# Kernel optimization log

Measured on AMD Instinct MI355X. Metric: run time of the kernel, lower is better.

Reference implementation:

```python
import jax, jax.numpy as jnp
import numpy as np

D_MODEL = 2048
N_HEADS = 16
N_KV_HEADS = 4
HEAD_DIM = 128
ROPE_THETA = 1000000.0
B, T = 2, 2048


def setup_inputs() -> dict:
    key = jax.random.key(0)
    ks = jax.random.split(key, 5)
    s_in = 1.0 / np.sqrt(D_MODEL)
    s_o = 1.0 / np.sqrt(N_HEADS * HEAD_DIM)
    return {
        "x": jax.random.normal(ks[0], (B, T, D_MODEL), jnp.float32),
        "w_q": jax.random.normal(ks[1], (N_HEADS * HEAD_DIM, D_MODEL), jnp.float32) * s_in,
        "w_k": jax.random.normal(ks[2], (N_KV_HEADS * HEAD_DIM, D_MODEL), jnp.float32) * s_in,
        "w_v": jax.random.normal(ks[3], (N_KV_HEADS * HEAD_DIM, D_MODEL), jnp.float32) * s_in,
        "w_o": jax.random.normal(ks[4], (D_MODEL, N_HEADS * HEAD_DIM), jnp.float32) * s_o,
    }


def _rope_cos_sin(T, dtype):
    # inv_freq over even dims, emb = concat(freqs, freqs) (HF/llama convention)
    inv_freq = 1.0 / (ROPE_THETA ** (jnp.arange(0, HEAD_DIM, 2, dtype=jnp.float32) / HEAD_DIM))
    freqs = jnp.arange(T, dtype=jnp.float32)[:, None] * inv_freq[None, :]  # [T, hd/2]
    emb = jnp.concatenate([freqs, freqs], axis=-1)  # [T, hd]
    return jnp.cos(emb).astype(dtype), jnp.sin(emb).astype(dtype)


def _rotate_half(x):
    x1, x2 = jnp.split(x, 2, axis=-1)
    return jnp.concatenate([-x2, x1], axis=-1)


def reference(x, w_q, w_k, w_v, w_o):
    B, T, D = x.shape
    # QKV projections (bias=False), split heads -> [B, H, T, hd]
    q = (x @ w_q.T).reshape(B, T, N_HEADS, HEAD_DIM).transpose(0, 2, 1, 3)
    k = (x @ w_k.T).reshape(B, T, N_KV_HEADS, HEAD_DIM).transpose(0, 2, 1, 3)
    v = (x @ w_v.T).reshape(B, T, N_KV_HEADS, HEAD_DIM).transpose(0, 2, 1, 3)
    # RoPE
    cos, sin = _rope_cos_sin(T, x.dtype)  # [T, hd]
    q = q * cos + _rotate_half(q) * sin
    k = k * cos + _rotate_half(k) * sin
    # GQA: expand kv heads (repeat_interleave over head dim)
    rep = N_HEADS // N_KV_HEADS
    k = jnp.repeat(k, rep, axis=1)
    v = jnp.repeat(v, rep, axis=1)
    # Eager attention: QK^T * scale + causal mask, softmax, PV
    scale = HEAD_DIM ** -0.5
    scores = jnp.einsum("bhtd,bhsd->bhts", q, k) * scale
    causal = jnp.tril(jnp.ones((T, T), dtype=bool))
    scores = jnp.where(causal[None, None], scores, jnp.finfo(scores.dtype).min)
    probs = jax.nn.softmax(scores, axis=-1)
    out = jnp.einsum("bhts,bhsd->bhtd", probs, v)  # [B, H, T, hd]
    out = out.transpose(0, 2, 1, 3).reshape(B, T, N_HEADS * HEAD_DIM)
    return out @ w_o.T
```

## Files before the change

kernel.cpp:

```cpp
#include <hip/hip_runtime.h>
#include <cstdint>
#include <cstddef>

typedef unsigned short u16;
typedef unsigned u32;
typedef unsigned long long u64;
typedef __attribute__((ext_vector_type(8))) short short8;
typedef __attribute__((ext_vector_type(4))) float f32x4;

#define T_SEQ 2048
#define DM    2048
#define NHEAD 16
#define NKV   4
#define HD    128
#define NEGBIG (-3.0e38f)
#define QSCALE 0.1275525165017459f
#define L2IF (-0.31143258583318043f)

__device__ __forceinline__ u16 f2bf(float f) {
  union { float f; unsigned u; } c; c.f = f;
  return (u16)((c.u + 0x7fffu + ((c.u >> 16) & 1u)) >> 16);
}
__device__ __forceinline__ float bf2f(u16 b) {
  union { float f; unsigned u; } c; c.u = ((unsigned)b) << 16;
  return c.f;
}
__device__ __forceinline__ void gl_lds16(const u16* g, u16* l) {
  __builtin_amdgcn_global_load_lds(
      (const __attribute__((address_space(1))) void*)g,
      (__attribute__((address_space(3))) void*)l, 16, 0, 0);
}

__global__ void castk_all(const float* __restrict__ x, const float* __restrict__ wq,
                          const float* __restrict__ wk, const float* __restrict__ wv,
                          const float* __restrict__ wo, u16* __restrict__ dst) {
  long long i4 = (long long)blockIdx.x * 256 + threadIdx.x;
  const float* src; long long off;
  if (i4 < (2LL << 20))                    { src = x;  off = i4; }
  else if (i4 < (3LL << 20))               { src = wq; off = i4 - (2LL << 20); }
  else if (i4 < (3LL << 20) + (1 << 18))   { src = wk; off = i4 - (3LL << 20); }
  else if (i4 < (3LL << 20) + (2 << 18))   { src = wv; off = i4 - (3LL << 20) - (1 << 18); }
  else                                     { src = wo; off = i4 - (3LL << 20) - (2 << 18); }
  float4 v = *(const float4*)(src + off * 4);
  u16* d = dst + i4 * 4;
  d[0] = f2bf(v.x); d[1] = f2bf(v.y); d[2] = f2bf(v.z); d[3] = f2bf(v.w);
}

__global__ void tabk(float2* __restrict__ Tab) {
  int idx = blockIdx.x * 256 + threadIdx.x;
  float ang = (float)(idx >> 6) * exp2f((float)(idx & 63) * L2IF);
  float sn, cs;
  sincosf(ang, &sn, &cs);
  Tab[idx] = make_float2(cs, sn);
}

__global__ void ropek(u16* __restrict__ buf, const float2* __restrict__ Tab) {
  int idx = blockIdx.x * 256 + threadIdx.x;
  int r = idx >> 6, i = idx & 63;
  int t = r & (T_SEQ - 1);
  float2 cs = Tab[(t << 6) + i];
  size_t base = (size_t)r * HD + i;
  float x1 = bf2f(buf[base]), x2 = bf2f(buf[base + 64]);
  buf[base]      = f2bf(x1 * cs.x - x2 * cs.y);
  buf[base + 64] = f2bf(x2 * cs.x + x1 * cs.y);
}

template <int MODE>
__global__ __launch_bounds__(256) void gemm_bt(
    const u16* __restrict__ A, const u16* __restrict__ Bm,
    void* __restrict__ Out0, u16* __restrict__ OutK, u16* __restrict__ OutV,
    int M, int N, int K) {
  __shared__ __align__(16) u16 As[2][128 * 32];
  __shared__ __align__(16) u16 Bs[2][128 * 32];
  const int tid = threadIdx.x;
  const int w = tid >> 6, l = tid & 63;
  const int lm = l & 15, q = l >> 4;
  const int chunk = gridDim.x >> 3;
  const int nid = (blockIdx.x & 7) * chunk + (blockIdx.x >> 3);
  const int nbx = N >> 7;
  const int by = nid / nbx, bx = nid - by * nbx;
  const int m0 = by * 128, n0 = bx * 128;
  const int mq = w & 1, nq = w >> 1;
  const u16* Ab = A + (size_t)m0 * K;
  const u16* Bb = Bm + (size_t)n0 * K;

  const int s0_ = w * 64 + l, s1_ = 256 + s0_;
  const int row0 = s0_ >> 2, sc0 = (((s0_ & 3) ^ ((s0_ >> 3) & 3))) * 8;
  const int row1 = s1_ >> 2, sc1 = (((s1_ & 3) ^ ((s1_ >> 3) & 3))) * 8;
  const int rs = (lm >> 1) & 3;

  f32x4 acc[4][4] = {};
  const int nk = K >> 5;

  gl_lds16(Ab + (size_t)row0 * K + sc0, &As[0][s0_ * 8]);
  gl_lds16(Bb + (size_t)row0 * K + sc0, &Bs[0][s0_ * 8]);
  gl_lds16(Ab + (size_t)row1 * K + sc1, &As[0][s1_ * 8]);
  gl_lds16(Bb + (size_t)row1 * K + sc1, &Bs[0][s1_ * 8]);
  __syncthreads();

  for (int ki = 0; ki < nk; ++ki) {
    const int bb = ki & 1;
    if (ki + 1 < nk) {
      const int k0 = (ki + 1) << 5;
      gl_lds16(Ab + (size_t)row0 * K + k0 + sc0, &As[bb ^ 1][s0_ * 8]);
      gl_lds16(Bb + (size_t)row0 * K + k0 + sc0, &Bs[bb ^ 1][s0_ * 8]);
      gl_lds16(Ab + (size_t)row1 * K + k0 + sc1, &As[bb ^ 1][s1_ * 8]);
      gl_lds16(Bb + (size_t)row1 * K + k0 + sc1, &Bs[bb ^ 1][s1_ * 8]);
    }
    short8 af[4], bf[4];
#pragma unroll
    for (int i = 0; i < 4; ++i) {
      af[i] = *(const short8*)(&As[bb][(mq * 64 + i * 16 + lm) * 32 + (q ^ rs) * 8]);
      bf[i] = *(const short8*)(&Bs[bb][(nq * 64 + i * 16 + lm) * 32 + (q ^ rs) * 8]);
    }
#pragma unroll
    for (int i = 0; i < 4; ++i)
#pragma unroll
      for (int j = 0; j < 4; ++j)
        acc[i][j] = __builtin_amdgcn_mfma_f32_16x16x32_bf16(af[i], bf[j], acc[i][j], 0, 0, 0);
    __syncthreads();
  }

#pragma unroll
  for (int i = 0; i < 4; ++i)
#pragma unroll
    for (int j = 0; j < 4; ++j)
#pragma unroll
      for (int r = 0; r < 4; ++r) {
        int m = m0 + mq * 64 + i * 16 + q * 4 + r;
        int n = n0 + nq * 64 + j * 16 + lm;
        float v = acc[i][j][r];
        if constexpr (MODE == 0) {
          ((float*)Out0)[(size_t)m * N + n] = v;
        } else {
          int b = m >> 11, t = m & (T_SEQ - 1);
          if (n < 2048) {
            int h = n >> 7, d = n & (HD - 1);
            ((u16*)Out0)[(((size_t)(b * NHEAD + h)) * T_SEQ + t) * HD + d] = f2bf(v * QSCALE);
          } else if (n < 2560) {
            int nn = n - 2048, h = nn >> 7, d = nn & (HD - 1);
            OutK[(((size_t)(b * NKV + h)) * T_SEQ + t) * HD + d] = f2bf(v);
          } else {
            int nn = n - 2560, h = nn >> 7, d = nn & (HD - 1);
            OutV[(((size_t)(b * NKV + h)) * HD + d) * T_SEQ + t] = f2bf(v);
          }
        }
      }
}

#define PSTRIDE 72
__global__ __launch_bounds__(256, 2) void attnk(
    const u16* __restrict__ Q, const u16* __restrict__ Kh,
    const u16* __restrict__ Vt, const float2* __restrict__ Tab,
    u16* __restrict__ Oa) {
  __shared__ __align__(16) u16 Ks[2][64 * 128];
  __shared__ __align__(16) u16 Vs[2][128 * 64];
  __shared__ __align__(16) u16 Pl[4][16 * PSTRIDE];
  const int tid = threadIdx.x;
  const int w = tid >> 6, l = tid & 63, lm = l & 15, q = l >> 4;

  const int wg = blockIdx.x;
  const int g = wg & 7, slot = wg >> 3;
  const int b = g >> 2, kvh = g & 3;
  const int h = kvh * 4 + (slot & 3);
  const int p = slot >> 2;

  const u16* Kb = Kh + ((size_t)(b * NKV + kvh)) * T_SEQ * HD;
  const u16* Vb = Vt + ((size_t)(b * NKV + kvh)) * HD * T_SEQ;
  u16* Pw = Pl[w];

  const int r16 = tid >> 4, c16 = tid & 15;
  const int r8  = tid >> 3, c8  = tid & 7;

#pragma unroll 1
  for (int half = 0; half < 2; ++half) {
    const int tile = half ? p : (31 - p);
    const int tbase = tile * 64 + w * 16;
    const u16* Qb = Q + (((size_t)(b * NHEAD + h)) * T_SEQ + tbase) * HD;

    short8 qa[4];
#pragma unroll
    for (int ks = 0; ks < 4; ++ks)
      qa[ks] = *(const short8*)(Qb + (size_t)lm * HD + ks * 32 + q * 8);

    {
      const float2* tb = Tab + (((size_t)(tbase + lm)) << 6) + q * 8;
#pragma unroll
      for (int ks = 0; ks < 2; ++ks) {
        short8 lo = qa[ks], hi = qa[ks + 2];
#pragma unroll
        for (int e = 0; e < 8; ++e) {
          float2 cs = tb[ks * 32 + e];
          float x1 = bf2f((u16)lo[e]), x2 = bf2f((u16)hi[e]);
          lo[e] = (short)f2bf(x1 * cs.x - x2 * cs.y);
          hi[e] = (short)f2bf(x2 * cs.x + x1 * cs.y);
        }
        qa[ks] = lo; qa[ks + 2] = hi;
      }
    }

    float m_i = NEGBIG, l_i = 0.f;
    f32x4 oacc[8] = {};
    const int nst = tile + 1;

    {
#pragma unroll
      for (int j = 0; j < 4; ++j) {
        int s = j * 16 + r16, gs = c16 ^ (s & 15);
        gl_lds16(Kb + (size_t)s * HD + gs * 8, &Ks[0][s * 128 + c16 * 8]);
      }
#pragma unroll
      for (int j = 0; j < 4; ++j) {
        int d = j * 32 + r8, gs = c8 ^ (d & 7);
        gl_lds16(Vb + (size_t)d * T_SEQ + gs * 8, &Vs[0][d * 64 + c8 * 8]);
      }
    }
    __syncthreads();

    for (int st = 0; st < nst; ++st) {
      const int bb = st & 1;
      if (st + 1 < nst) {
        const int s0n = (st + 1) * 64;
#pragma unroll
        for (int j = 0; j < 4; ++j) {
          int s = j * 16 + r16, gs = c16 ^ (s & 15);
          gl_lds16(Kb + (size_t)(s0n + s) * HD + gs * 8, &Ks[bb ^ 1][s * 128 + c16 * 8]);
        }
#pragma unroll
        for (int j = 0; j < 4; ++j) {
          int d = j * 32 + r8, gs = c8 ^ (d & 7);
          gl_lds16(Vb + (size_t)d * T_SEQ + s0n + gs * 8, &Vs[bb ^ 1][d * 64 + c8 * 8]);
        }
      }

      f32x4 sacc[4] = {};
#pragma unroll
      for (int ks = 0; ks < 4; ++ks)
#pragma unroll
        for (int nt = 0; nt < 4; ++nt) {
          short8 kb = *(const short8*)(&Ks[bb][(nt * 16 + lm) * 128 + ((ks * 4 + q) ^ lm) * 8]);
          sacc[nt] = __builtin_amdgcn_mfma_f32_16x16x32_bf16(kb, qa[ks], sacc[nt], 0, 0, 0);
        }

      const bool diag = (st == nst - 1);
      const int s0 = st * 64;
      float mx = NEGBIG;
#pragma unroll
      for (int nt = 0; nt < 4; ++nt)
#pragma unroll
        for (int j = 0; j < 4; ++j) {
          float v = sacc[nt][j];
          if (diag) {
            int s_abs = s0 + nt * 16 + q * 4 + j;
            if (s_abs > tbase + lm) v = NEGBIG;
            sacc[nt][j] = v;
          }
          mx = fmaxf(mx, v);
        }
      mx = fmaxf(mx, __shfl_xor(mx, 16, 64));
      mx = fmaxf(mx, __shfl_xor(mx, 32, 64));
      if (__any(mx > m_i + 8.0f)) {
        float mnew = fmaxf(m_i, mx);
        float alpha = exp2f(m_i - mnew);
        m_i = mnew;
        l_i *= alpha;
#pragma unroll
        for (int dt = 0; dt < 8; ++dt)
#pragma unroll
          for (int j = 0; j < 4; ++j) oacc[dt][j] *= alpha;
      }
      float sum = 0.f;
#pragma unroll
      for (int nt = 0; nt < 4; ++nt) {
        float e0 = exp2f(sacc[nt][0] - m_i), e1 = exp2f(sacc[nt][1] - m_i);
        float e2 = exp2f(sacc[nt][2] - m_i), e3 = exp2f(sacc[nt][3] - m_i);
        sum += (e0 + e1) + (e2 + e3);
        u32 lo32 = __builtin_amdgcn_perm(__float_as_uint(e1), __float_as_uint(e0), 0x07060302u);
        u32 hi32 = __builtin_amdgcn_perm(__float_as_uint(e3), __float_as_uint(e2), 0x07060302u);
        *(u64*)(Pw + lm * PSTRIDE + nt * 16 + q * 4) = ((u64)hi32 << 32) | lo32;
      }
      sum += __shfl_xor(sum, 16, 64);
      sum += __shfl_xor(sum, 32, 64);
      l_i += sum;

      asm volatile("" ::: "memory");

#pragma unroll
      for (int ks = 0; ks < 2; ++ks) {
        short8 pa = *(const short8*)(Pw + lm * PSTRIDE + ks * 32 + q * 8);
#pragma unroll
        for (int dt = 0; dt < 8; ++dt) {
          short8 vb = *(const short8*)(
              &Vs[bb][(dt * 16 + lm) * 64 + ((ks * 4 + q) ^ (lm & 7)) * 8]);
          oacc[dt] = __builtin_amdgcn_mfma_f32_16x16x32_bf16(vb, pa, oacc[dt], 0, 0, 0);
        }
      }
      __syncthreads();
    }

    float inv = 1.0f / l_i;
    int t = tbase + lm;
#pragma unroll
    for (int dt = 0; dt < 8; ++dt) {
      u16 ok[4];
#pragma unroll
      for (int j = 0; j < 4; ++j) ok[j] = f2bf(oacc[dt][j] * inv);
      *(u64*)(Oa + ((size_t)(b * T_SEQ + t)) * (NHEAD * HD) + h * HD + dt * 16 + q * 4) =
          (u64)ok[0] | ((u64)ok[1] << 16) | ((u64)ok[2] << 32) | ((u64)ok[3] << 48);
    }
  }
}

extern "C" void kernel_launch(void* const* d_in, const int* in_sizes, int n_in,
                              void* d_out, int out_size, void* d_ws, size_t ws_size,
                              hipStream_t stream) {
  const float* x  = (const float*)d_in[0];
  const float* wq = (const float*)d_in[1];
  const float* wk = (const float*)d_in[2];
  const float* wv = (const float*)d_in[3];
  const float* wo = (const float*)d_in[4];
  float* out = (float*)d_out;

  u16* ws  = (u16*)d_ws;
  u16* xb  = ws;
  u16* wqb = xb  + (8u << 20);
  u16* wkb = wqb + (4u << 20);
  u16* wvb = wkb + (1u << 20);
  u16* wob = wvb + (1u << 20);
  u16* Qb  = wob + (4u << 20);
  u16* Kb  = Qb  + (8u << 20);
  u16* Vtb = Kb  + (2u << 20);
  u16* Ab  = xb;
  float2* tab = (float2*)wkb;

  castk_all<<<18432, 256, 0, stream>>>(x, wq, wk, wv, wo, ws);

  gemm_bt<3><<<768, 256, 0, stream>>>(xb, wqb, Qb, Kb, Vtb, 4096, 3072, 2048);

  tabk<<<512, 256, 0, stream>>>(tab);
  ropek<<<4096, 256, 0, stream>>>(Kb, tab);

  attnk<<<512, 256, 0, stream>>>(Qb, Kb, Vtb, tab, Ab);

  gemm_bt<0><<<512, 256, 0, stream>>>(Ab, wob, out, nullptr, nullptr, 4096, 2048, 2048);
}
```

Measured before the change: 291.3 us.

## Split attention into one tile per block with smaller KV blocks and fuse rope table

The attention kernel no longer pairs a long and a short query tile per block. It now launches one block per query tile (1024 blocks), uses 32-row KV stages with smaller LDS buffers, and raises the occupancy hint to 4 blocks per CU, with swizzle and P-stride reworked to match. The separate RoPE table kernel is folded into the K-rope kernel, which computes sin/cos inline and writes the table for the attention kernel. The aims are more parallelism and occupancy plus one fewer launch. The cost is load imbalance from causal tiles of different lengths, and twice as many sync and softmax steps per unit of work.

```diff
diff --git a/kernel.cpp b/kernel.cpp
--- a/kernel.cpp
+++ b/kernel.cpp
@@ -46,23 +46,18 @@
   d[0] = f2bf(v.x); d[1] = f2bf(v.y); d[2] = f2bf(v.z); d[3] = f2bf(v.w);
 }
 
-__global__ void tabk(float2* __restrict__ Tab) {
-  int idx = blockIdx.x * 256 + threadIdx.x;
-  float ang = (float)(idx >> 6) * exp2f((float)(idx & 63) * L2IF);
-  float sn, cs;
-  sincosf(ang, &sn, &cs);
-  Tab[idx] = make_float2(cs, sn);
-}
-
-__global__ void ropek(u16* __restrict__ buf, const float2* __restrict__ Tab) {
+__global__ void ropek(u16* __restrict__ buf, float2* __restrict__ Tab) {
   int idx = blockIdx.x * 256 + threadIdx.x;
   int r = idx >> 6, i = idx & 63;
   int t = r & (T_SEQ - 1);
-  float2 cs = Tab[(t << 6) + i];
+  float ang = (float)t * exp2f((float)i * L2IF);
+  float sn, cs;
+  sincosf(ang, &sn, &cs);
+  if (r < T_SEQ) Tab[(r << 6) + i] = make_float2(cs, sn);
   size_t base = (size_t)r * HD + i;
   float x1 = bf2f(buf[base]), x2 = bf2f(buf[base + 64]);
-  buf[base]      = f2bf(x1 * cs.x - x2 * cs.y);
-  buf[base + 64] = f2bf(x2 * cs.x + x1 * cs.y);
+  buf[base]      = f2bf(x1 * cs - x2 * sn);
+  buf[base + 64] = f2bf(x2 * cs + x1 * sn);
 }
 
 template <int MODE>
@@ -148,13 +143,14 @@
       }
 }
 
-#define PSTRIDE 72
-__global__ __launch_bounds__(256, 2) void attnk(
+#define KVB 32
+#define PSTRIDE 40
+__global__ __launch_bounds__(256, 4) void attnk(
     const u16* __restrict__ Q, const u16* __restrict__ Kh,
     const u16* __restrict__ Vt, const float2* __restrict__ Tab,
     u16* __restrict__ Oa) {
-  __shared__ __align__(16) u16 Ks[2][64 * 128];
-  __shared__ __align__(16) u16 Vs[2][128 * 64];
+  __shared__ __align__(16) u16 Ks[2][KVB * 128];
+  __shared__ __align__(16) u16 Vs[2][128 * KVB];
   __shared__ __align__(16) u16 Pl[4][16 * PSTRIDE];
   const int tid = threadIdx.x;
   const int w = tid >> 6, l = tid & 63, lm = l & 15, q = l >> 4;
@@ -163,151 +159,136 @@
   const int g = wg & 7, slot = wg >> 3;
   const int b = g >> 2, kvh = g & 3;
   const int h = kvh * 4 + (slot & 3);
-  const int p = slot >> 2;
+  const int tile = 31 - (slot >> 2);
 
   const u16* Kb = Kh + ((size_t)(b * NKV + kvh)) * T_SEQ * HD;
   const u16* Vb = Vt + ((size_t)(b * NKV + kvh)) * HD * T_SEQ;
   u16* Pw = Pl[w];
 
-  const int r16 = tid >> 4, c16 = tid & 15;
-  const int r8  = tid >> 3, c8  = tid & 7;
-
-#pragma unroll 1
-  for (int half = 0; half < 2; ++half) {
-    const int tile = half ? p : (31 - p);
-    const int tbase = tile * 64 + w * 16;
-    const u16* Qb = Q + (((size_t)(b * NHEAD + h)) * T_SEQ + tbase) * HD;
-
-    short8 qa[4];
+  const int krow = tid >> 4;
+  const int kc   = tid & 15;
+  const int kcol = (kc ^ (krow & 15)) * 8;
+  const int vrow = tid >> 2;
+  const int vc   = tid & 3;
+  const int vcol = (vc ^ ((tid >> 3) & 3)) * 8;
+
+  const int tbase = tile * 64 + w * 16;
+  const u16* Qb = Q + (((size_t)(b * NHEAD + h)) * T_SEQ + tbase) * HD;
+
+  short8 qa[4];
+#pragma unroll
+  for (int ks = 0; ks < 4; ++ks)
+    qa[ks] = *(const short8*)(Qb + (size_t)lm * HD + ks * 32 + q * 8);
+
+  {
+    const float2* tb = Tab + (((size_t)(tbase + lm)) << 6) + q * 8;
+#pragma unroll
+    for (int ks = 0; ks < 2; ++ks) {
+      short8 lo = qa[ks], hi = qa[ks + 2];
+#pragma unroll
+      for (int e = 0; e < 8; ++e) {
+        float2 cs = tb[ks * 32 + e];
+        float x1 = bf2f((u16)lo[e]), x2 = bf2f((u16)hi[e]);
+        lo[e] = (short)f2bf(x1 * cs.x - x2 * cs.y);
+        hi[e] = (short)f2bf(x2 * cs.x + x1 * cs.y);
+      }
+      qa[ks] = lo; qa[ks + 2] = hi;
+    }
+  }
+
+  float m_i = NEGBIG, l_i = 0.f;
+  f32x4 oacc[8] = {};
+  const int nst = 2 * tile + 2;
+
+  gl_lds16(Kb + (size_t)krow * HD + kcol, &Ks[0][krow * 128 + kc * 8]);
+  gl_lds16(Kb + (size_t)(krow + 16) * HD + kcol, &Ks[0][(krow + 16) * 128 + kc * 8]);
+  gl_lds16(Vb + (size_t)vrow * T_SEQ + vcol, &Vs[0][vrow * KVB + vc * 8]);
+  gl_lds16(Vb + (size_t)(vrow + 64) * T_SEQ + vcol, &Vs[0][(vrow + 64) * KVB + vc * 8]);
+  __syncthreads();
+
+  for (int st = 0; st < nst; ++st) {
+    const int bb = st & 1;
+    const int s0 = st * KVB;
+    if (st + 1 < nst) {
+      const int s0n = s0 + KVB;
+      gl_lds16(Kb + (size_t)(s0n + krow) * HD + kcol, &Ks[bb ^ 1][krow * 128 + kc * 8]);
+      gl_lds16(Kb + (size_t)(s0n + krow + 16) * HD + kcol, &Ks[bb ^ 1][(krow + 16) * 128 + kc * 8]);
+      gl_lds16(Vb + (size_t)vrow * T_SEQ + s0n + vcol, &Vs[bb ^ 1][vrow * KVB + vc * 8]);
+      gl_lds16(Vb + (size_t)(vrow + 64) * T_SEQ + s0n + vcol, &Vs[bb ^ 1][(vrow + 64) * KVB + vc * 8]);
+    }
+
+    f32x4 sacc[2] = {};
 #pragma unroll
     for (int ks = 0; ks < 4; ++ks)
-      qa[ks] = *(const short8*)(Qb + (size_t)lm * HD + ks * 32 + q * 8);
+#pragma unroll
+      for (int nt = 0; nt < 2; ++nt) {
+        short8 kb = *(const short8*)(&Ks[bb][(nt * 16 + lm) * 128 + ((ks * 4 + q) ^ lm) * 8]);
+        sacc[nt] = __builtin_amdgcn_mfma_f32_16x16x32_bf16(kb, qa[ks], sacc[nt], 0, 0, 0);
+      }
+
+    const bool diag = (s0 + KVB - 1 > tbase);
+    float mx = NEGBIG;
+#pragma unroll
+    for (int nt = 0; nt < 2; ++nt)
+#pragma unroll
+      for (int j = 0; j < 4; ++j) {
+        float v = sacc[nt][j];
+        if (diag) {
+          int s_abs = s0 + nt * 16 + q * 4 + j;
+          if (s_abs > tbase + lm) v = NEGBIG;
+          sacc[nt][j] = v;
+        }
+        mx = fmaxf(mx, v);
+      }
+    mx = fmaxf(mx, __shfl_xor(mx, 16, 64));
+    mx = fmaxf(mx, __shfl_xor(mx, 32, 64));
+    if (__any(mx > m_i + 8.0f)) {
+      float mnew = fmaxf(m_i, mx);
+      float alpha = exp2f(m_i - mnew);
+      m_i = mnew;
+      l_i *= alpha;
+#pragma unroll
+      for (int dt = 0; dt < 8; ++dt)
+#pragma unroll
+        for (int j = 0; j < 4; ++j) oacc[dt][j] *= alpha;
+    }
+    float sum = 0.f;
+#pragma unroll
+    for (int nt = 0; nt < 2; ++nt) {
+      float e0 = exp2f(sacc[nt][0] - m_i), e1 = exp2f(sacc[nt][1] - m_i);
+      float e2 = exp2f(sacc[nt][2] - m_i), e3 = exp2f(sacc[nt][3] - m_i);
+      sum += (e0 + e1) + (e2 + e3);
+      u32 lo32 = __builtin_amdgcn_perm(__float_as_uint(e1), __float_as_uint(e0), 0x07060302u);
+      u32 hi32 = __builtin_amdgcn_perm(__float_as_uint(e3), __float_as_uint(e2), 0x07060302u);
+      *(u64*)(Pw + lm * PSTRIDE + nt * 16 + q * 4) = ((u64)hi32 << 32) | lo32;
+    }
+    sum += __shfl_xor(sum, 16, 64);
+    sum += __shfl_xor(sum, 32, 64);
+    l_i += sum;
+
+    asm volatile("" ::: "memory");
 
     {
-      const float2* tb = Tab + (((size_t)(tbase + lm)) << 6) + q * 8;
-#pragma unroll
-      for (int ks = 0; ks < 2; ++ks) {
-        short8 lo = qa[ks], hi = qa[ks + 2];
-#pragma unroll
-        for (int e = 0; e < 8; ++e) {
-          float2 cs = tb[ks * 32 + e];
-          float x1 = bf2f((u16)lo[e]), x2 = bf2f((u16)hi[e]);
-          lo[e] = (short)f2bf(x1 * cs.x - x2 * cs.y);
-          hi[e] = (short)f2bf(x2 * cs.x + x1 * cs.y);
-        }
-        qa[ks] = lo; qa[ks + 2] = hi;
-      }
-    }
-
-    float m_i = NEGBIG, l_i = 0.f;
-    f32x4 oacc[8] = {};
-    const int nst = tile + 1;
-
-    {
-#pragma unroll
-      for (int j = 0; j < 4; ++j) {
-        int s = j * 16 + r16, gs = c16 ^ (s & 15);
-        gl_lds16(Kb + (size_t)s * HD + gs * 8, &Ks[0][s * 128 + c16 * 8]);
-      }
-#pragma unroll
-      for (int j = 0; j < 4; ++j) {
-        int d = j * 32 + r8, gs = c8 ^ (d & 7);
-        gl_lds16(Vb + (size_t)d * T_SEQ + gs * 8, &Vs[0][d * 64 + c8 * 8]);
+      short8 pa = *(const short8*)(Pw + lm * PSTRIDE + q * 8);
+#pragma unroll
+      for (int dt = 0; dt < 8; ++dt) {
+        short8 vb = *(const short8*)(
+            &Vs[bb][(dt * 16 + lm) * KVB + (q ^ ((lm >> 1) & 3)) * 8]);
+        oacc[dt] = __builtin_amdgcn_mfma_f32_16x16x32_bf16(vb, pa, oacc[dt], 0, 0, 0);
       }
     }
     __syncthreads();
-
-    for (int st = 0; st < nst; ++st) {
-      const int bb = st & 1;
-      if (st + 1 < nst) {
-        const int s0n = (st + 1) * 64;
-#pragma unroll
-        for (int j = 0; j < 4; ++j) {
-          int s = j * 16 + r16, gs = c16 ^ (s & 15);
-          gl_lds16(Kb + (size_t)(s0n + s) * HD + gs * 8, &Ks[bb ^ 1][s * 128 + c16 * 8]);
-        }
-#pragma unroll
-        for (int j = 0; j < 4; ++j) {
-          int d = j * 32 + r8, gs = c8 ^ (d & 7);
-          gl_lds16(Vb + (size_t)d * T_SEQ + s0n + gs * 8, &Vs[bb ^ 1][d * 64 + c8 * 8]);
-        }
-      }
-
-      f32x4 sacc[4] = {};
-#pragma unroll
-      for (int ks = 0; ks < 4; ++ks)
-#pragma unroll
-        for (int nt = 0; nt < 4; ++nt) {
-          short8 kb = *(const short8*)(&Ks[bb][(nt * 16 + lm) * 128 + ((ks * 4 + q) ^ lm) * 8]);
-          sacc[nt] = __builtin_amdgcn_mfma_f32_16x16x32_bf16(kb, qa[ks], sacc[nt], 0, 0, 0);
-        }
-
-      const bool diag = (st == nst - 1);
-      const int s0 = st * 64;
-      float mx = NEGBIG;
-#pragma unroll
-      for (int nt = 0; nt < 4; ++nt)
-#pragma unroll
-        for (int j = 0; j < 4; ++j) {
-          float v = sacc[nt][j];
-          if (diag) {
-            int s_abs = s0 + nt * 16 + q * 4 + j;
-            if (s_abs > tbase + lm) v = NEGBIG;
-            sacc[nt][j] = v;
-          }
-          mx = fmaxf(mx, v);
-        }
-      mx = fmaxf(mx, __shfl_xor(mx, 16, 64));
-      mx = fmaxf(mx, __shfl_xor(mx, 32, 64));
-      if (__any(mx > m_i + 8.0f)) {
-        float mnew = fmaxf(m_i, mx);
-        float alpha = exp2f(m_i - mnew);
-        m_i = mnew;
-        l_i *= alpha;
-#pragma unroll
-        for (int dt = 0; dt < 8; ++dt)
-#pragma unroll
-          for (int j = 0; j < 4; ++j) oacc[dt][j] *= alpha;
-      }
-      float sum = 0.f;
-#pragma unroll
-      for (int nt = 0; nt < 4; ++nt) {
-        float e0 = exp2f(sacc[nt][0] - m_i), e1 = exp2f(sacc[nt][1] - m_i);
-        float e2 = exp2f(sacc[nt][2] - m_i), e3 = exp2f(sacc[nt][3] - m_i);
-        sum += (e0 + e1) + (e2 + e3);
-        u32 lo32 = __builtin_amdgcn_perm(__float_as_uint(e1), __float_as_uint(e0), 0x07060302u);
-        u32 hi32 = __builtin_amdgcn_perm(__float_as_uint(e3), __float_as_uint(e2), 0x07060302u);
-        *(u64*)(Pw + lm * PSTRIDE + nt * 16 + q * 4) = ((u64)hi32 << 32) | lo32;
-      }
-      sum += __shfl_xor(sum, 16, 64);
-      sum += __shfl_xor(sum, 32, 64);
-      l_i += sum;
-
-      asm volatile("" ::: "memory");
-
-#pragma unroll
-      for (int ks = 0; ks < 2; ++ks) {
-        short8 pa = *(const short8*)(Pw + lm * PSTRIDE + ks * 32 + q * 8);
-#pragma unroll
-        for (int dt = 0; dt < 8; ++dt) {
-          short8 vb = *(const short8*)(
-              &Vs[bb][(dt * 16 + lm) * 64 + ((ks * 4 + q) ^ (lm & 7)) * 8]);
-          oacc[dt] = __builtin_amdgcn_mfma_f32_16x16x32_bf16(vb, pa, oacc[dt], 0, 0, 0);
-        }
-      }
-      __syncthreads();
-    }
-
-    float inv = 1.0f / l_i;
-    int t = tbase + lm;
-#pragma unroll
-    for (int dt = 0; dt < 8; ++dt) {
-      u16 ok[4];
-#pragma unroll
-      for (int j = 0; j < 4; ++j) ok[j] = f2bf(oacc[dt][j] * inv);
-      *(u64*)(Oa + ((size_t)(b * T_SEQ + t)) * (NHEAD * HD) + h * HD + dt * 16 + q * 4) =
-          (u64)ok[0] | ((u64)ok[1] << 16) | ((u64)ok[2] << 32) | ((u64)ok[3] << 48);
-    }
+  }
+
+  float inv = 1.0f / l_i;
+  int t = tbase + lm;
+#pragma unroll
+  for (int dt = 0; dt < 8; ++dt) {
+    u16 ok[4];
+#pragma unroll
+    for (int j = 0; j < 4; ++j) ok[j] = f2bf(oacc[dt][j] * inv);
+    *(u64*)(Oa + ((size_t)(b * T_SEQ + t)) * (NHEAD * HD) + h * HD + dt * 16 + q * 4) =
+        (u64)ok[0] | ((u64)ok[1] << 16) | ((u64)ok[2] << 32) | ((u64)ok[3] << 48);
   }
 }
 
@@ -337,10 +318,9 @@
 
   gemm_bt<3><<<768, 256, 0, stream>>>(xb, wqb, Qb, Kb, Vtb, 4096, 3072, 2048);
 
-  tabk<<<512, 256, 0, stream>>>(tab);
   ropek<<<4096, 256, 0, stream>>>(Kb, tab);
 
-  attnk<<<512, 256, 0, stream>>>(Qb, Kb, Vtb, tab, Ab);
+  attnk<<<1024, 256, 0, stream>>>(Qb, Kb, Vtb, tab, Ab);
 
   gemm_bt<0><<<512, 256, 0, stream>>>(Ab, wob, out, nullptr, nullptr, 4096, 2048, 2048);
 }
```

Result: slower. 305.0 us (+4.7%).

## Give each attention wave 32 query rows and fold RoPE table build into ropek

Applied to the files above, without the earlier changes.

The attention kernel now runs 128-thread blocks of two waves, and each wave processes two 16-row query groups, so every K and V fragment read from LDS feeds two MFMAs. The intent is to halve LDS traffic per unit of compute. The cost is doubled accumulator registers (oacc and sacc) and fewer waves per block to hide latency. Separately, the sin/cos table is now computed inside the K RoPE kernel, which writes the table for the first 2048 rows, removing one launch.

```diff
diff --git a/kernel.cpp b/kernel.cpp
--- a/kernel.cpp
+++ b/kernel.cpp
@@ -46,23 +46,18 @@
   d[0] = f2bf(v.x); d[1] = f2bf(v.y); d[2] = f2bf(v.z); d[3] = f2bf(v.w);
 }
 
-__global__ void tabk(float2* __restrict__ Tab) {
-  int idx = blockIdx.x * 256 + threadIdx.x;
-  float ang = (float)(idx >> 6) * exp2f((float)(idx & 63) * L2IF);
-  float sn, cs;
-  sincosf(ang, &sn, &cs);
-  Tab[idx] = make_float2(cs, sn);
-}
-
-__global__ void ropek(u16* __restrict__ buf, const float2* __restrict__ Tab) {
+__global__ void ropek(u16* __restrict__ buf, float2* __restrict__ Tab) {
   int idx = blockIdx.x * 256 + threadIdx.x;
   int r = idx >> 6, i = idx & 63;
   int t = r & (T_SEQ - 1);
-  float2 cs = Tab[(t << 6) + i];
+  float ang = (float)t * exp2f((float)i * L2IF);
+  float sn, cs;
+  sincosf(ang, &sn, &cs);
+  if (r < T_SEQ) Tab[(r << 6) + i] = make_float2(cs, sn);
   size_t base = (size_t)r * HD + i;
   float x1 = bf2f(buf[base]), x2 = bf2f(buf[base + 64]);
-  buf[base]      = f2bf(x1 * cs.x - x2 * cs.y);
-  buf[base + 64] = f2bf(x2 * cs.x + x1 * cs.y);
+  buf[base]      = f2bf(x1 * cs - x2 * sn);
+  buf[base + 64] = f2bf(x2 * cs + x1 * sn);
 }
 
 template <int MODE>
@@ -149,13 +144,13 @@
 }
 
 #define PSTRIDE 72
-__global__ __launch_bounds__(256, 2) void attnk(
+__global__ __launch_bounds__(128) void attnk(
     const u16* __restrict__ Q, const u16* __restrict__ Kh,
     const u16* __restrict__ Vt, const float2* __restrict__ Tab,
     u16* __restrict__ Oa) {
   __shared__ __align__(16) u16 Ks[2][64 * 128];
   __shared__ __align__(16) u16 Vs[2][128 * 64];
-  __shared__ __align__(16) u16 Pl[4][16 * PSTRIDE];
+  __shared__ __align__(16) u16 Pl[2][32 * PSTRIDE];
   const int tid = threadIdx.x;
   const int w = tid >> 6, l = tid & 63, lm = l & 15, q = l >> 4;
 
@@ -175,19 +170,23 @@
 #pragma unroll 1
   for (int half = 0; half < 2; ++half) {
     const int tile = half ? p : (31 - p);
-    const int tbase = tile * 64 + w * 16;
-    const u16* Qb = Q + (((size_t)(b * NHEAD + h)) * T_SEQ + tbase) * HD;
-
-    short8 qa[4];
-#pragma unroll
-    for (int ks = 0; ks < 4; ++ks)
-      qa[ks] = *(const short8*)(Qb + (size_t)lm * HD + ks * 32 + q * 8);
-
-    {
-      const float2* tb = Tab + (((size_t)(tbase + lm)) << 6) + q * 8;
+    const int tbase = tile * 64;
+    const int qrb = tbase + w * 32;
+    const u16* Qb = Q + (((size_t)(b * NHEAD + h)) * T_SEQ + qrb) * HD;
+
+    short8 qa[2][4];
+#pragma unroll
+    for (int rg = 0; rg < 2; ++rg)
+#pragma unroll
+      for (int ks = 0; ks < 4; ++ks)
+        qa[rg][ks] = *(const short8*)(Qb + (size_t)(rg * 16 + lm) * HD + ks * 32 + q * 8);
+
+#pragma unroll
+    for (int rg = 0; rg < 2; ++rg) {
+      const float2* tb = Tab + (((size_t)(qrb + rg * 16 + lm)) << 6) + q * 8;
 #pragma unroll
       for (int ks = 0; ks < 2; ++ks) {
-        short8 lo = qa[ks], hi = qa[ks + 2];
+        short8 lo = qa[rg][ks], hi = qa[rg][ks + 2];
 #pragma unroll
         for (int e = 0; e < 8; ++e) {
           float2 cs = tb[ks * 32 + e];
@@ -195,118 +194,132 @@
           lo[e] = (short)f2bf(x1 * cs.x - x2 * cs.y);
           hi[e] = (short)f2bf(x2 * cs.x + x1 * cs.y);
         }
-        qa[ks] = lo; qa[ks + 2] = hi;
-      }
-    }
-
-    float m_i = NEGBIG, l_i = 0.f;
-    f32x4 oacc[8] = {};
+        qa[rg][ks] = lo; qa[rg][ks + 2] = hi;
+      }
+    }
+
+    float m_i[2] = {NEGBIG, NEGBIG}, l_i[2] = {0.f, 0.f};
+    f32x4 oacc[2][8] = {};
     const int nst = tile + 1;
 
-    {
-#pragma unroll
-      for (int j = 0; j < 4; ++j) {
-        int s = j * 16 + r16, gs = c16 ^ (s & 15);
-        gl_lds16(Kb + (size_t)s * HD + gs * 8, &Ks[0][s * 128 + c16 * 8]);
-      }
-#pragma unroll
-      for (int j = 0; j < 4; ++j) {
-        int d = j * 32 + r8, gs = c8 ^ (d & 7);
-        gl_lds16(Vb + (size_t)d * T_SEQ + gs * 8, &Vs[0][d * 64 + c8 * 8]);
-      }
+#pragma unroll
+    for (int j = 0; j < 8; ++j) {
+      int s = j * 8 + r16, gs = c16 ^ (s & 15);
+      gl_lds16(Kb + (size_t)s * HD + gs * 8, &Ks[0][s * 128 + c16 * 8]);
+    }
+#pragma unroll
+    for (int j = 0; j < 8; ++j) {
+      int d = j * 16 + r8, gs = c8 ^ (d & 7);
+      gl_lds16(Vb + (size_t)d * T_SEQ + gs * 8, &Vs[0][d * 64 + c8 * 8]);
     }
     __syncthreads();
 
     for (int st = 0; st < nst; ++st) {
       const int bb = st & 1;
+      const int s0 = st * 64;
       if (st + 1 < nst) {
-        const int s0n = (st + 1) * 64;
-#pragma unroll
-        for (int j = 0; j < 4; ++j) {
-          int s = j * 16 + r16, gs = c16 ^ (s & 15);
+        const int s0n = s0 + 64;
+#pragma unroll
+        for (int j = 0; j < 8; ++j) {
+          int s = j * 8 + r16, gs = c16 ^ (s & 15);
           gl_lds16(Kb + (size_t)(s0n + s) * HD + gs * 8, &Ks[bb ^ 1][s * 128 + c16 * 8]);
         }
 #pragma unroll
-        for (int j = 0; j < 4; ++j) {
-          int d = j * 32 + r8, gs = c8 ^ (d & 7);
+        for (int j = 0; j < 8; ++j) {
+          int d = j * 16 + r8, gs = c8 ^ (d & 7);
           gl_lds16(Vb + (size_t)d * T_SEQ + s0n + gs * 8, &Vs[bb ^ 1][d * 64 + c8 * 8]);
         }
       }
 
-      f32x4 sacc[4] = {};
+      f32x4 sacc[2][4] = {};
 #pragma unroll
       for (int ks = 0; ks < 4; ++ks)
 #pragma unroll
         for (int nt = 0; nt < 4; ++nt) {
           short8 kb = *(const short8*)(&Ks[bb][(nt * 16 + lm) * 128 + ((ks * 4 + q) ^ lm) * 8]);
-          sacc[nt] = __builtin_amdgcn_mfma_f32_16x16x32_bf16(kb, qa[ks], sacc[nt], 0, 0, 0);
-        }
-
-      const bool diag = (st == nst - 1);
-      const int s0 = st * 64;
-      float mx = NEGBIG;
-#pragma unroll
-      for (int nt = 0; nt < 4; ++nt)
-#pragma unroll
-        for (int j = 0; j < 4; ++j) {
-          float v = sacc[nt][j];
-          if (diag) {
-            int s_abs = s0 + nt * 16 + q * 4 + j;
-            if (s_abs > tbase + lm) v = NEGBIG;
-            sacc[nt][j] = v;
+          sacc[0][nt] = __builtin_amdgcn_mfma_f32_16x16x32_bf16(kb, qa[0][ks], sacc[0][nt], 0, 0, 0);
+          sacc[1][nt] = __builtin_amdgcn_mfma_f32_16x16x32_bf16(kb, qa[1][ks], sacc[1][nt], 0, 0, 0);
+        }
+
+      const bool diag = (s0 + 63 > qrb);
+      float mx[2] = {NEGBIG, NEGBIG};
+#pragma unroll
+      for (int rg = 0; rg < 2; ++rg) {
+#pragma unroll
+        for (int nt = 0; nt < 4; ++nt)
+#pragma unroll
+          for (int j = 0; j < 4; ++j) {
+            float v = sacc[rg][nt][j];
+            if (diag) {
+              int s_abs = s0 + nt * 16 + q * 4 + j;
+              if (s_abs > qrb + rg * 16 + lm) v = NEGBIG;
+              sacc[rg][nt][j] = v;
+            }
+            mx[rg] = fmaxf(mx[rg], v);
           }
-          mx = fmaxf(mx, v);
-        }
-      mx = fmaxf(mx, __shfl_xor(mx, 16, 64));
-      mx = fmaxf(mx, __shfl_xor(mx, 32, 64));
-      if (__any(mx > m_i + 8.0f)) {
-        float mnew = fmaxf(m_i, mx);
-        float alpha = exp2f(m_i - mnew);
-        m_i = mnew;
-        l_i *= alpha;
-#pragma unroll
-        for (int dt = 0; dt < 8; ++dt)
-#pragma unroll
-          for (int j = 0; j < 4; ++j) oacc[dt][j] *= alpha;
-      }
-      float sum = 0.f;
-#pragma unroll
-      for (int nt = 0; nt < 4; ++nt) {
-        float e0 = exp2f(sacc[nt][0] - m_i), e1 = exp2f(sacc[nt][1] - m_i);
-        float e2 = exp2f(sacc[nt][2] - m_i), e3 = exp2f(sacc[nt][3] - m_i);
-        sum += (e0 + e1) + (e2 + e3);
-        u32 lo32 = __builtin_amdgcn_perm(__float_as_uint(e1), __float_as_uint(e0), 0x07060302u);
-        u32 hi32 = __builtin_amdgcn_perm(__float_as_uint(e3), __float_as_uint(e2), 0x07060302u);
-        *(u64*)(Pw + lm * PSTRIDE + nt * 16 + q * 4) = ((u64)hi32 << 32) | lo32;
-      }
-      sum += __shfl_xor(sum, 16, 64);
-      sum += __shfl_xor(sum, 32, 64);
-      l_i += sum;
+        mx[rg] = fmaxf(mx[rg], __shfl_xor(mx[rg], 16, 64));
+        mx[rg] = fmaxf(mx[rg], __shfl_xor(mx[rg], 32, 64));
+      }
+      bool bump = (mx[0] > m_i[0] + 8.0f) || (mx[1] > m_i[1] + 8.0f);
+      if (__any(bump)) {
+#pragma unroll
+        for (int rg = 0; rg < 2; ++rg) {
+          float mnew = fmaxf(m_i[rg], mx[rg]);
+          float alpha = exp2f(m_i[rg] - mnew);
+          m_i[rg] = mnew;
+          l_i[rg] *= alpha;
+#pragma unroll
+          for (int dt = 0; dt < 8; ++dt)
+#pragma unroll
+            for (int j = 0; j < 4; ++j) oacc[rg][dt][j] *= alpha;
+        }
+      }
+#pragma unroll
+      for (int rg = 0; rg < 2; ++rg) {
+        float sum = 0.f;
+#pragma unroll
+        for (int nt = 0; nt < 4; ++nt) {
+          float e0 = exp2f(sacc[rg][nt][0] - m_i[rg]), e1 = exp2f(sacc[rg][nt][1] - m_i[rg]);
+          float e2 = exp2f(sacc[rg][nt][2] - m_i[rg]), e3 = exp2f(sacc[rg][nt][3] - m_i[rg]);
+          sum += (e0 + e1) + (e2 + e3);
+          u32 lo32 = __builtin_amdgcn_perm(__float_as_uint(e1), __float_as_uint(e0), 0x07060302u);
+          u32 hi32 = __builtin_amdgcn_perm(__float_as_uint(e3), __float_as_uint(e2), 0x07060302u);
+          *(u64*)(Pw + (rg * 16 + lm) * PSTRIDE + nt * 16 + q * 4) = ((u64)hi32 << 32) | lo32;
+        }
+        sum += __shfl_xor(sum, 16, 64);
+        sum += __shfl_xor(sum, 32, 64);
+        l_i[rg] += sum;
+      }
 
       asm volatile("" ::: "memory");
 
 #pragma unroll
       for (int ks = 0; ks < 2; ++ks) {
-        short8 pa = *(const short8*)(Pw + lm * PSTRIDE + ks * 32 + q * 8);
+        short8 pa0 = *(const short8*)(Pw + (0 + lm) * PSTRIDE + ks * 32 + q * 8);
+        short8 pa1 = *(const short8*)(Pw + (16 + lm) * PSTRIDE + ks * 32 + q * 8);
 #pragma unroll
         for (int dt = 0; dt < 8; ++dt) {
           short8 vb = *(const short8*)(
               &Vs[bb][(dt * 16 + lm) * 64 + ((ks * 4 + q) ^ (lm & 7)) * 8]);
-          oacc[dt] = __builtin_amdgcn_mfma_f32_16x16x32_bf16(vb, pa, oacc[dt], 0, 0, 0);
+          oacc[0][dt] = __builtin_amdgcn_mfma_f32_16x16x32_bf16(vb, pa0, oacc[0][dt], 0, 0, 0);
+          oacc[1][dt] = __builtin_amdgcn_mfma_f32_16x16x32_bf16(vb, pa1, oacc[1][dt], 0, 0, 0);
         }
       }
       __syncthreads();
     }
 
-    float inv = 1.0f / l_i;
-    int t = tbase + lm;
-#pragma unroll
-    for (int dt = 0; dt < 8; ++dt) {
-      u16 ok[4];
-#pragma unroll
-      for (int j = 0; j < 4; ++j) ok[j] = f2bf(oacc[dt][j] * inv);
-      *(u64*)(Oa + ((size_t)(b * T_SEQ + t)) * (NHEAD * HD) + h * HD + dt * 16 + q * 4) =
-          (u64)ok[0] | ((u64)ok[1] << 16) | ((u64)ok[2] << 32) | ((u64)ok[3] << 48);
+#pragma unroll
+    for (int rg = 0; rg < 2; ++rg) {
+      float inv = 1.0f / l_i[rg];
+      int t = qrb + rg * 16 + lm;
+#pragma unroll
+      for (int dt = 0; dt < 8; ++dt) {
+        u16 ok[4];
+#pragma unroll
+        for (int j = 0; j < 4; ++j) ok[j] = f2bf(oacc[rg][dt][j] * inv);
+        *(u64*)(Oa + ((size_t)(b * T_SEQ + t)) * (NHEAD * HD) + h * HD + dt * 16 + q * 4) =
+            (u64)ok[0] | ((u64)ok[1] << 16) | ((u64)ok[2] << 32) | ((u64)ok[3] << 48);
+      }
     }
   }
 }
@@ -337,10 +350,9 @@
 
   gemm_bt<3><<<768, 256, 0, stream>>>(xb, wqb, Qb, Kb, Vtb, 4096, 3072, 2048);
 
-  tabk<<<512, 256, 0, stream>>>(tab);
   ropek<<<4096, 256, 0, stream>>>(Kb, tab);
 
-  attnk<<<512, 256, 0, stream>>>(Qb, Kb, Vtb, tab, Ab);
+  attnk<<<512, 128, 0, stream>>>(Qb, Kb, Vtb, tab, Ab);
 
   gemm_bt<0><<<512, 256, 0, stream>>>(Ab, wob, out, nullptr, nullptr, 4096, 2048, 2048);
 }
```

Result: slower. 336.2 us (+15.4%).
